# Optimization experiments

Hardware: AMD Instinct MI355X
Metric: run time of the kernel (lower is better)

Reference implementation:

```python
import jax, jax.numpy as jnp
import numpy as np
from jax import lax

HIDDEN = 7168
Q_LORA = 1536
N_HEAD = 64
HEAD_DIM = 128
ROPE_DIM = 64
TOPK = 2048
T = 4096
ROPE_BASE = 10000.0
LN_EPS = 1e-6
NEG_INF = -1e30


def _apply_rope_interleaved(x, cos, sin):
    # x: [..., ROPE_DIM], cos/sin broadcastable to [..., ROPE_DIM//2]
    x1 = x[..., 0::2]
    x2 = x[..., 1::2]
    o1 = x1 * cos - x2 * sin
    o2 = x1 * sin + x2 * cos
    out = jnp.stack([o1, o2], axis=-1)  # interleave back
    return out.reshape(x.shape)


def setup_inputs() -> dict:
    key = jax.random.key(0)
    ks = jax.random.split(key, 6)
    hidden_states = jax.random.normal(ks[0], (T, HIDDEN), dtype=jnp.float32)
    qr = jax.random.normal(ks[1], (T, Q_LORA), dtype=jnp.float32)
    positions = jnp.arange(T, dtype=jnp.int32)
    # learned parameters (stored [in, out] so fwd is x @ W)
    Wq_b = jax.random.normal(ks[2], (Q_LORA, N_HEAD * HEAD_DIM), dtype=jnp.float32) * 0.02
    Wk = jax.random.normal(ks[3], (HIDDEN, HEAD_DIM), dtype=jnp.float32) * 0.02
    Wproj = jax.random.normal(ks[4], (HIDDEN, N_HEAD), dtype=jnp.float32) * 0.02
    k_norm_gamma = jnp.ones((HEAD_DIM,), dtype=jnp.float32)
    k_norm_beta = jnp.zeros((HEAD_DIM,), dtype=jnp.float32)
    return {
        'hidden_states': hidden_states,
        'qr': qr,
        'positions': positions,
        'Wq_b': Wq_b,
        'Wk': Wk,
        'Wproj': Wproj,
        'k_norm_gamma': k_norm_gamma,
        'k_norm_beta': k_norm_beta,
    }


def _indexer_forward(hidden_states, qr, positions, Wq_b, Wk, Wproj, gamma, beta):
    # q projection: [T, n_head * head_dim] -> [T, H, D]
    q = (qr @ Wq_b).reshape(T, N_HEAD, HEAD_DIM)
    q_pe, q_nope = q[..., :ROPE_DIM], q[..., ROPE_DIM:]

    # k projection + LayerNorm (eps=1e-6)
    k = hidden_states @ Wk  # [T, D]
    mu = jnp.mean(k, axis=-1, keepdims=True)
    var = jnp.mean(jnp.square(k - mu), axis=-1, keepdims=True)
    k = (k - mu) * lax.rsqrt(var + LN_EPS) * gamma + beta
    k_pe, k_nope = k[..., :ROPE_DIM], k[..., ROPE_DIM:]

    # RoPE (interleaved / GPT-J style, as used by DeepSeek rotary)
    inv_freq = 1.0 / (ROPE_BASE ** (jnp.arange(0, ROPE_DIM, 2, dtype=jnp.float32) / ROPE_DIM))
    ang = positions.astype(jnp.float32)[:, None] * inv_freq[None, :]  # [T, R/2]
    cos, sin = jnp.cos(ang), jnp.sin(ang)
    q_pe = _apply_rope_interleaved(q_pe, cos[:, None, :], sin[:, None, :])  # [T, H, R]
    k_pe = _apply_rope_interleaved(k_pe, cos, sin)  # [T, R]

    q_full = jnp.concatenate([q_pe, q_nope], axis=-1)  # [T, H, D]
    k_full = jnp.concatenate([k_pe, k_nope], axis=-1)  # [T, D]

    # per-token per-head weights, scaled by head_dim**-0.5 * n_head**-0.5
    w = (hidden_states @ Wproj) * (HEAD_DIM ** -0.5) * (N_HEAD ** -0.5)  # [T, H]

    # lightning-indexer score: sum_h w[t,h] * relu(q[t,h,:] . k[s,:])
    # scan over heads so live intermediate is a single [T, T] matrix
    qh_all = jnp.transpose(q_full, (1, 0, 2))  # [H, T, D]
    wh_all = w.T  # [H, T]

    def body(acc, hw):
        qh, wh = hw  # [T, D], [T]
        acc = acc + wh[:, None] * jax.nn.relu(qh @ k_full.T)
        return acc, None

    scores, _ = lax.scan(body, jnp.zeros((T, T), dtype=jnp.float32), (qh_all, wh_all))

    # causal mask over key positions, then select top-k keys per query
    causal = positions[:, None] >= positions[None, :]
    masked = jnp.where(causal, scores, NEG_INF)
    topk_vals, topk_idx = lax.top_k(masked, TOPK)  # [T, TOPK]
    return topk_vals, topk_idx


def reference(hidden_states, qr, positions, Wq_b, Wk, Wproj, k_norm_gamma, k_norm_beta):
    return _indexer_forward(hidden_states, qr, positions, Wq_b, Wk, Wproj, k_norm_gamma, k_norm_beta)
```

## Files before the change

kernel.cpp:

```cpp
#include <hip/hip_runtime.h>
#include <stdint.h>

#define TT 4096
#define HID 7168
#define QL 1536
#define NH 64
#define HD 128
#define QD 8192
#define KTOP 2048
#define WSCALE 0.011048543456039806f

typedef _Float16 f16;
typedef uint16_t u16;
typedef unsigned u32;
typedef __attribute__((ext_vector_type(4))) float f32x4;
typedef __attribute__((ext_vector_type(16))) float f32x16;
typedef __attribute__((ext_vector_type(8))) _Float16 f16x8;
typedef __attribute__((ext_vector_type(4))) _Float16 f16x4;

__device__ __forceinline__ void lds_load16(const void* g, void* l) {
  __builtin_amdgcn_global_load_lds(
      (const __attribute__((address_space(1))) unsigned*)g,
      (__attribute__((address_space(3))) unsigned*)l, 16, 0, 0);
}

__device__ __forceinline__ u16 f16_bits(f16 h) {
  union { f16 h; u16 u; } c; c.h = h; return c.u;
}
__device__ __forceinline__ float f16_from_bits(u16 u) {
  union { u16 u; f16 h; } c; c.u = u; return (float)c.h;
}

__global__ void tcvt(const float* __restrict__ in, f16* __restrict__ out,
                     int R, int C, int ostride, int orow0) {
  __shared__ float tile[32][33];
  int cb = blockIdx.x * 32, rb = blockIdx.y * 32;
  int tx = threadIdx.x & 31, ty = threadIdx.x >> 5;
  for (int i = 0; i < 32; i += 8)
    tile[ty + i][tx] = in[(size_t)(rb + ty + i) * C + cb + tx];
  __syncthreads();
  for (int i = 0; i < 32; i += 8)
    out[(size_t)(cb + ty + i + orow0) * ostride + rb + tx] = (f16)tile[tx][ty + i];
}

__launch_bounds__(256, 2)
__global__ void gemm_q(const float* __restrict__ A, const f16* __restrict__ B, f16* __restrict__ C) {
  __shared__ __align__(16) f16 As[128 * 32];
  __shared__ __align__(16) f16 Bs[128 * 32];
  int tid = threadIdx.x, lane = tid & 63, wave = tid >> 6;
  int bm = blockIdx.y << 7, bn = blockIdx.x << 7;
  int wm = (wave & 1) << 6, wn = (wave >> 1) << 6;
  const f16* gb = B + (size_t)(bn + (tid >> 2)) * QL + (tid & 3) * 8;
  f16* lB = Bs + wave * 512;
  int ar = tid >> 3, ac = (tid & 7) * 4;
  f32x4 acc[4][4] = {};
  for (int k0 = 0; k0 < QL; k0 += 32) {
    __syncthreads();
#pragma unroll
    for (int i = 0; i < 4; i++) {
      float4 v = *(const float4*)(A + (size_t)(bm + ar + i * 32) * QL + k0 + ac);
      f16x4 h = {(f16)v.x, (f16)v.y, (f16)v.z, (f16)v.w};
      *(f16x4*)(As + (ar + i * 32) * 32 + ac) = h;
    }
    lds_load16(gb + k0, lB);
    lds_load16(gb + (size_t)64 * QL + k0, lB + 2048);
    __syncthreads();
    int ro = lane & 15, ko = (lane >> 4) << 3;
    f16x8 af[4], bf[4];
#pragma unroll
    for (int i = 0; i < 4; i++) af[i] = *(const f16x8*)(As + (wm + i * 16 + ro) * 32 + ko);
#pragma unroll
    for (int i = 0; i < 4; i++) bf[i] = *(const f16x8*)(Bs + (wn + i * 16 + ro) * 32 + ko);
#pragma unroll
    for (int mi = 0; mi < 4; mi++)
#pragma unroll
      for (int ni = 0; ni < 4; ni++)
        acc[mi][ni] = __builtin_amdgcn_mfma_f32_16x16x32_f16(af[mi], bf[ni], acc[mi][ni], 0, 0, 0);
  }
  int cr = (lane >> 4) << 2, cc = lane & 15;
#pragma unroll
  for (int mi = 0; mi < 4; mi++)
#pragma unroll
    for (int ni = 0; ni < 4; ni++) {
      int row = bm + wm + mi * 16 + cr;
      int col = bn + wn + ni * 16 + cc;
      f16* cp = C + (size_t)row * QD + col;
#pragma unroll
      for (int r = 0; r < 4; r++) cp[(size_t)r * QD] = (f16)acc[mi][ni][r];
    }
}

__launch_bounds__(256, 2)
__global__ void gemm_kw(const float* __restrict__ A, const f16* __restrict__ B,
                        float* __restrict__ kraw, float* __restrict__ wout) {
  __shared__ __align__(16) f16 As[64 * 64];
  __shared__ __align__(16) f16 Bs[64 * 64];
  int tid = threadIdx.x, lane = tid & 63, wave = tid >> 6;
  int bm = blockIdx.y << 6, bn = blockIdx.x << 6;
  int wm = (wave & 1) << 5, wn = (wave >> 1) << 5;
  const f16* gb = B + (size_t)(bn + (tid >> 3)) * HID + (tid & 7) * 8;
  f16* lB = Bs + wave * 512;
  int ar = tid >> 4, ac = (tid & 15) * 4;
  f32x4 acc[2][2] = {};
  for (int k0 = 0; k0 < HID; k0 += 64) {
    __syncthreads();
#pragma unroll
    for (int i = 0; i < 4; i++) {
      float4 v = *(const float4*)(A + (size_t)(bm + ar + i * 16) * HID + k0 + ac);
      f16x4 h = {(f16)v.x, (f16)v.y, (f16)v.z, (f16)v.w};
      *(f16x4*)(As + (ar + i * 16) * 64 + ac) = h;
    }
    lds_load16(gb + k0, lB);
    lds_load16(gb + (size_t)32 * HID + k0, lB + 2048);
    __syncthreads();
    int ro = lane & 15, ko = (lane >> 4) << 3;
    f16x8 af[2][2], bf[2][2];
#pragma unroll
    for (int i = 0; i < 2; i++)
#pragma unroll
      for (int kk = 0; kk < 2; kk++) {
        af[i][kk] = *(const f16x8*)(As + (wm + i * 16 + ro) * 64 + kk * 32 + ko);
        bf[i][kk] = *(const f16x8*)(Bs + (wn + i * 16 + ro) * 64 + kk * 32 + ko);
      }
#pragma unroll
    for (int mi = 0; mi < 2; mi++)
#pragma unroll
      for (int ni = 0; ni < 2; ni++)
#pragma unroll
        for (int kk = 0; kk < 2; kk++)
          acc[mi][ni] = __builtin_amdgcn_mfma_f32_16x16x32_f16(af[mi][kk], bf[ni][kk], acc[mi][ni], 0, 0, 0);
  }
  int cr = (lane >> 4) << 2, cc = lane & 15;
#pragma unroll
  for (int mi = 0; mi < 2; mi++)
#pragma unroll
    for (int ni = 0; ni < 2; ni++) {
      int row = bm + wm + mi * 16 + cr;
      int col = bn + wn + ni * 16 + cc;
#pragma unroll
      for (int r = 0; r < 4; r++) {
        float v = acc[mi][ni][r];
        int rr = row + r;
        if (col < HD) kraw[(size_t)rr * HD + col] = v;
        else          wout[(size_t)rr * NH + (col - HD)] = v * WSCALE;
      }
    }
}

__global__ void ln_rope(const float* __restrict__ kraw, const int* __restrict__ pos,
                        const float* __restrict__ gamma, const float* __restrict__ beta,
                        f16* __restrict__ k16) {
  int row = (blockIdx.x << 2) + (threadIdx.x >> 6);
  int lane = threadIdx.x & 63;
  const float* kr = kraw + (size_t)row * HD;
  float2 x = ((const float2*)kr)[lane];
  float s = x.x + x.y, s2 = x.x * x.x + x.y * x.y;
  for (int off = 32; off; off >>= 1) { s += __shfl_down(s, off); s2 += __shfl_down(s2, off); }
  s = __shfl(s, 0); s2 = __shfl(s2, 0);
  float mu = s * (1.f / 128.f);
  float var = s2 * (1.f / 128.f) - mu * mu;
  float inv = rsqrtf(var + 1e-6f);
  float y0 = (x.x - mu) * inv * gamma[lane * 2] + beta[lane * 2];
  float y1 = (x.y - mu) * inv * gamma[lane * 2 + 1] + beta[lane * 2 + 1];
  float o0 = y0, o1 = y1;
  if (lane < 32) {
    float p = (float)pos[row];
    float invf = exp2f(-(float)lane * 0.41524101185942813f);
    float ang = p * invf;
    float sn, cn;
    sincosf(ang, &sn, &cn);
    o0 = y0 * cn - y1 * sn;
    o1 = y0 * sn + y1 * cn;
  }
  k16[(size_t)row * HD + 2 * lane] = (f16)o0;
  k16[(size_t)row * HD + 2 * lane + 1] = (f16)o1;
}

template <int N>
__device__ __forceinline__ void sort_and_store(u32* key, int tid, int t, float* out) {
  constexpr int V = N / 256;
  u32 v[V];
#pragma unroll
  for (int r = 0; r < V; r += 4) {
    uint4 q4 = *(const uint4*)(key + tid * V + r);
    v[r] = ~q4.x; v[r + 1] = ~q4.y; v[r + 2] = ~q4.z; v[r + 3] = ~q4.w;
  }
#pragma unroll
  for (int k = 2; k <= N; k <<= 1) {
#pragma unroll
    for (int j = k >> 1; j > 0; j >>= 1) {
      if (j >= 64 * V) {
#pragma unroll
        for (int r = 0; r < V; r += 4) {
          uint4 q4 = {v[r], v[r + 1], v[r + 2], v[r + 3]};
          *(uint4*)(key + tid * V + r) = q4;
        }
        __syncthreads();
        for (int m = tid; m < N / 2; m += 256) {
          int i = ((m & ~(j - 1)) << 1) | (m & (j - 1));
          int l = i | j;
          bool up = ((i & k) == 0);
          u32 a = key[i], b = key[l];
          if (up ? (a > b) : (a < b)) { key[i] = b; key[l] = a; }
        }
        __syncthreads();
#pragma unroll
        for (int r = 0; r < V; r += 4) {
          uint4 q4 = *(const uint4*)(key + tid * V + r);
          v[r] = q4.x; v[r + 1] = q4.y; v[r + 2] = q4.z; v[r + 3] = q4.w;
        }
      } else if (j >= V) {
        int lanej = j / V;
        bool takeMin = (((tid & lanej) == 0) == (((tid * V) & k) == 0));
#pragma unroll
        for (int r = 0; r < V; r++) {
          u32 o = __shfl_xor(v[r], lanej, 64);
          u32 mn = min(v[r], o), mx = max(v[r], o);
          v[r] = takeMin ? mn : mx;
        }
      } else {
#pragma unroll
        for (int r = 0; r < V; r++) {
          if ((r & j) == 0) {
            bool up = (((tid * V + r) & k) == 0);
            u32 a = v[r], b = v[r | j];
            u32 mn = min(a, b), mx = max(a, b);
            v[r] = up ? mn : mx;
            v[r | j] = up ? mx : mn;
          }
        }
      }
    }
  }
  if (tid * V < KTOP) {
    float* ov = out + (size_t)t * KTOP + tid * V;
    float* oi = out + (size_t)TT * KTOP + (size_t)t * KTOP + tid * V;
#pragma unroll
    for (int r = 0; r < V; r++) {
      u32 kv = ~v[r];
      u32 mono = kv >> 16;
      float val;
      if (mono == 0u) {
        val = -1e30f;
      } else {
        u16 hb = (u16)((mono & 0x8000u) ? (mono ^ 0x8000u) : (mono ^ 0xFFFFu));
        val = f16_from_bits(hb);
      }
      ov[r] = val;
      oi[r] = (float)(0xFFFFu - (kv & 0xFFFFu));
    }
  }
}

__launch_bounds__(256, 3)
__global__ void scores_topk(const f16* __restrict__ q16, const f16* __restrict__ k16,
                            const float* __restrict__ w, const int* __restrict__ pos,
                            float* __restrict__ out) {
  int t = blockIdx.x;
  int tid = threadIdx.x, lane = tid & 63, wave = tid >> 6;
  __shared__ __align__(16) unsigned char smem[49408];
  f16* ks = (f16*)smem;
  f16* qk = (f16*)(smem + 32768);
  u32* key = (u32*)(smem + 32768);
  float* css = (float*)(smem + 49152);

  {
    const f16* qrow = q16 + (size_t)t * QD;
#pragma unroll
    for (int j = 0; j < 4; j++) {
      int u = j * 256 + tid;
      int kg = u >> 6, h = u & 63;
      lds_load16(qrow + h * 128 + kg * 8, qk + (size_t)(j * 256 + wave * 64) * 8);
    }
    if (tid < 32) {
      float invf = exp2f(-(float)tid * 0.41524101185942813f);
      float ang = (float)pos[t] * invf;
      float sn, cn;
      sincosf(ang, &sn, &cn);
      css[tid] = cn;
      css[32 + tid] = sn;
    }
  }
  __syncthreads();
#pragma unroll
  for (int i = 0; i < 8; i++) {
    int p = tid + (i << 8);
    int h = p >> 5, l = p & 31;
    int d = l * 2;
    int base = ((d >> 3) * 64 + h) * 8 + (d & 7);
    float q0 = (float)qk[base], q1 = (float)qk[base + 1];
    float cn = css[l], sn = css[32 + l];
    qk[base] = (f16)(q0 * cn - q1 * sn);
    qk[base + 1] = (f16)(q0 * sn + q1 * cn);
  }
  __syncthreads();
  f16x8 afr[2][8];
  {
    int m = lane & 31;
#pragma unroll
    for (int mi = 0; mi < 2; mi++)
#pragma unroll
      for (int kk = 0; kk < 8; kk++) {
        int kg = kk * 2 + (lane >> 5);
        afr[mi][kk] = *(const f16x8*)(qk + (size_t)(kg * 64 + mi * 32 + m) * 8);
      }
  }
  float wreg[32];
  {
    int hf = lane >> 5;
    const float* wr = w + (size_t)t * 64;
#pragma unroll
    for (int mi = 0; mi < 2; mi++)
#pragma unroll
      for (int r = 0; r < 16; r++)
        wreg[mi * 16 + r] = wr[mi * 32 + (r & 3) + ((r >> 2) << 3) + (hf << 2)];
  }
  __syncthreads();

  int nsort = (t <= 2047) ? 2048 : 4096;
  for (int s = tid; s < nsort; s += 256)
    key[s] = 0xFFFFu - (u32)s;

  int ntile = (t >> 7) + 1;
  int sw = wave << 5;
  for (int st = 0; st < ntile; st++) {
    int s0 = st << 7;
    __syncthreads();
    {
      const f16* kb = k16 + (size_t)s0 * HD;
#pragma unroll
      for (int j = 0; j < 8; j++) {
        int u = j * 256 + tid;
        int kg = u >> 7, s = u & 127;
        lds_load16(kb + s * HD + kg * 8, ks + (size_t)(j * 256 + wave * 64) * 8);
      }
    }
    __syncthreads();
    f32x16 acc0 = {}, acc1 = {};
    int nlo = lane & 31;
#pragma unroll
    for (int kk = 0; kk < 8; kk++) {
      int kg = kk * 2 + (lane >> 5);
      f16x8 bfr = *(const f16x8*)(ks + (size_t)(kg * 128 + sw + nlo) * 8);
      acc0 = __builtin_amdgcn_mfma_f32_32x32x16_f16(afr[0][kk], bfr, acc0, 0, 0, 0);
      acc1 = __builtin_amdgcn_mfma_f32_32x32x16_f16(afr[1][kk], bfr, acc1, 0, 0, 0);
    }
    float partial = 0.f;
#pragma unroll
    for (int r = 0; r < 16; r++) {
      partial += wreg[r] * fmaxf(acc0[r], 0.f);
      partial += wreg[16 + r] * fmaxf(acc1[r], 0.f);
    }
    partial += __shfl_xor(partial, 32);
    int s = s0 + sw + nlo;
    if (lane < 32 && s <= t) {
      if (!(partial == partial)) partial = 0.f;
      partial = fminf(fmaxf(partial, -60000.f), 60000.f);
      u16 hb = f16_bits((f16)partial);
      u32 m = (hb & 0x8000u) ? (u32)(hb ^ 0xFFFFu) : (u32)(hb | 0x8000u);
      key[s] = (m << 16) | (0xFFFFu - (u32)s);
    }
  }
  __syncthreads();

  if (t <= 2047) sort_and_store<2048>(key, tid, t, out);
  else           sort_and_store<4096>(key, tid, t, out);
}

extern "C" void kernel_launch(void* const* d_in, const int* in_sizes, int n_in,
                              void* d_out, int out_size, void* d_ws, size_t ws_size,
                              hipStream_t stream) {
  const float* hs = (const float*)d_in[0];
  const float* qr = (const float*)d_in[1];
  const int* pos = (const int*)d_in[2];
  const float* Wq = (const float*)d_in[3];
  const float* Wk = (const float*)d_in[4];
  const float* Wp = (const float*)d_in[5];
  const float* gamma = (const float*)d_in[6];
  const float* beta = (const float*)d_in[7];
  char* ws = (char*)d_ws;
  float* kraw = (float*)ws;
  float* wsc = (float*)(ws + 2097152);
  f16* k16 = (f16*)(ws + 3145728);
  f16* kwT = (f16*)(ws + 4194304);
  f16* wqT = (f16*)(ws + 6946816);
  f16* q16 = (f16*)(ws + 32112640);

  tcvt<<<dim3(256, 48), dim3(256), 0, stream>>>(Wq, wqT, QL, QD, QL, 0);
  tcvt<<<dim3(4, 224), dim3(256), 0, stream>>>(Wk, kwT, HID, HD, HID, 0);
  tcvt<<<dim3(2, 224), dim3(256), 0, stream>>>(Wp, kwT, HID, NH, HID, HD);
  gemm_kw<<<dim3(3, 64), dim3(256), 0, stream>>>(hs, kwT, kraw, wsc);
  ln_rope<<<dim3(1024), dim3(256), 0, stream>>>(kraw, pos, gamma, beta, k16);
  gemm_q<<<dim3(64, 32), dim3(256), 0, stream>>>(qr, wqT, q16);
  scores_topk<<<dim3(4096), dim3(256), 0, stream>>>(q16, k16, wsc, pos, (float*)d_out);
}
```

Measured before the change: 846.5 us.

## Split fused scores+topk into tiled score GEMM, separate RoPE, and top-k kernels

The per-query fused kernel, which reloaded every K tile for each query row, is replaced by three kernels. A separate pass applies RoPE to q in place. A 2D-tiled kernel then computes 32 queries by 256 keys, holding K fragments in registers, double-buffering per-head q slices through LDS, and writing causal f16 scores to a packed triangular buffer. A final top-k kernel reads those scores back and runs the existing bitonic sort. This raises K reuse and MFMA density, at the cost of extra launches and a global round trip for the score matrix. The score buffer reuses the workspace region of the transposed weights.

```diff
diff --git a/kernel.cpp b/kernel.cpp
--- a/kernel.cpp
+++ b/kernel.cpp
@@ -29,6 +29,11 @@
 }
 __device__ __forceinline__ float f16_from_bits(u16 u) {
   union { u16 u; f16 h; } c; c.u = u; return (float)c.h;
+}
+
+__device__ __forceinline__ size_t soff(int t) {
+  int b = t >> 7, r = t & 127;
+  return (size_t)128u * ((size_t)(b + 1) * (size_t)(64 * b + r));
 }
 
 __global__ void tcvt(const float* __restrict__ in, f16* __restrict__ out,
@@ -176,6 +181,127 @@
   k16[(size_t)row * HD + 2 * lane + 1] = (f16)o1;
 }
 
+__global__ void rope_q(f16* __restrict__ q16, const int* __restrict__ pos) {
+  int t = blockIdx.x, tid = threadIdx.x;
+  __shared__ float cs[64];
+  if (tid < 32) {
+    float invf = exp2f(-(float)tid * 0.41524101185942813f);
+    float ang = (float)pos[t] * invf;
+    float sn, cn;
+    sincosf(ang, &sn, &cn);
+    cs[tid] = cn;
+    cs[32 + tid] = sn;
+  }
+  __syncthreads();
+  f16* row = q16 + (size_t)t * QD;
+#pragma unroll
+  for (int it = 0; it < 2; it++) {
+    int u = it * 256 + tid;
+    int h = u >> 3, c = u & 7;
+    f16* p = row + h * HD + c * 8;
+    f16x8 v = *(f16x8*)p;
+#pragma unroll
+    for (int j = 0; j < 4; j++) {
+      int l = c * 4 + j;
+      float cn = cs[l], sn = cs[32 + l];
+      float x = (float)v[2 * j], y = (float)v[2 * j + 1];
+      v[2 * j] = (f16)(x * cn - y * sn);
+      v[2 * j + 1] = (f16)(x * sn + y * cn);
+    }
+    *(f16x8*)p = v;
+  }
+}
+
+__launch_bounds__(256, 3)
+__global__ void scores2(const f16* __restrict__ q16, const f16* __restrict__ k16,
+                        const float* __restrict__ w, f16* __restrict__ S) {
+  int kt0 = blockIdx.x << 8;
+  int qt0 = blockIdx.y << 5;
+  if (kt0 > qt0 + 31) return;
+  int tid = threadIdx.x, l = tid & 63, wid = tid >> 6;
+  int q = l & 31, half = l >> 5;
+  __shared__ __align__(16) f16 smem_q[8192];
+  __shared__ float w_lds[2048];
+
+  for (int i = tid; i < 2048; i += 256) {
+    int hh = i & 63, qq = i >> 6;
+    w_lds[hh * 32 + qq] = w[(size_t)(qt0 + qq) * NH + hh];
+  }
+  f16x8 kfr[2][8];
+  {
+    const f16* kb = k16 + (size_t)(kt0 + wid * 64 + q) * HD + half * 8;
+#pragma unroll
+    for (int mt = 0; mt < 2; mt++)
+#pragma unroll
+      for (int kk = 0; kk < 8; kk++)
+        kfr[mt][kk] = *(const f16x8*)(kb + mt * 32 * HD + kk * 16);
+  }
+  const f16* qbase = q16 + (size_t)qt0 * QD;
+#pragma unroll
+  for (int p = 0; p < 2; p++) {
+    int u = p * 256 + tid;
+    lds_load16(qbase + (size_t)(u & 31) * QD + (u >> 5) * 8, smem_q + u * 8);
+  }
+  f32x16 s0 = {}, s1 = {};
+  __syncthreads();
+
+  for (int h = 0; h < NH; h++) {
+    if (h < NH - 1) {
+      const f16* src = qbase + (h + 1) * HD;
+      f16* dst = smem_q + ((h + 1) & 1) * 4096;
+#pragma unroll
+      for (int p = 0; p < 2; p++) {
+        int u = p * 256 + tid;
+        lds_load16(src + (size_t)(u & 31) * QD + (u >> 5) * 8, dst + u * 8);
+      }
+    }
+    const f16* qb = smem_q + (h & 1) * 4096;
+    f32x16 a0 = {}, a1 = {};
+#pragma unroll
+    for (int kk = 0; kk < 8; kk++) {
+      f16x8 qf = *(const f16x8*)(qb + ((kk * 2 + half) * 32 + q) * 8);
+      a0 = __builtin_amdgcn_mfma_f32_32x32x16_f16(kfr[0][kk], qf, a0, 0, 0, 0);
+      a1 = __builtin_amdgcn_mfma_f32_32x32x16_f16(kfr[1][kk], qf, a1, 0, 0, 0);
+    }
+    float wv = w_lds[h * 32 + q];
+#pragma unroll
+    for (int r = 0; r < 16; r++) {
+      s0[r] += wv * fmaxf(a0[r], 0.f);
+      s1[r] += wv * fmaxf(a1[r], 0.f);
+    }
+    __syncthreads();
+  }
+
+  f16* st = smem_q;
+#pragma unroll
+  for (int mt = 0; mt < 2; mt++)
+#pragma unroll
+    for (int r = 0; r < 16; r++) {
+      int m = (r & 3) + ((r >> 2) << 3) + half * 4;
+      int sl = wid * 64 + mt * 32 + m;
+      float v = mt ? s1[r] : s0[r];
+      if (!(v == v)) v = 0.f;
+      v = fminf(fmaxf(v, -60000.f), 60000.f);
+      u32 byte = (u32)(q * 512 + sl * 2) ^ (u32)((q & 7) << 4);
+      *(f16*)((char*)st + byte) = (f16)v;
+    }
+  __syncthreads();
+  {
+    int rq = tid >> 3, c = tid & 7;
+    int t = qt0 + rq;
+    size_t base = soff(t) + (size_t)kt0;
+    bool hi = (t - kt0) >= 128;
+#pragma unroll
+    for (int j = 0; j < 4; j++) {
+      if (c < 4 || hi) {
+        u32 byte = (u32)(rq * 512 + c * 64 + j * 16) ^ (u32)((rq & 7) << 4);
+        uint4 v = *(uint4*)((char*)st + byte);
+        *(uint4*)(S + base + c * 32 + j * 8) = v;
+      }
+    }
+  }
+}
+
 template <int N>
 __device__ __forceinline__ void sort_and_store(u32* key, int tid, int t, float* out) {
   constexpr int V = N / 256;
@@ -252,117 +378,31 @@
   }
 }
 
-__launch_bounds__(256, 3)
-__global__ void scores_topk(const f16* __restrict__ q16, const f16* __restrict__ k16,
-                            const float* __restrict__ w, const int* __restrict__ pos,
-                            float* __restrict__ out) {
-  int t = blockIdx.x;
-  int tid = threadIdx.x, lane = tid & 63, wave = tid >> 6;
-  __shared__ __align__(16) unsigned char smem[49408];
-  f16* ks = (f16*)smem;
-  f16* qk = (f16*)(smem + 32768);
-  u32* key = (u32*)(smem + 32768);
-  float* css = (float*)(smem + 49152);
-
-  {
-    const f16* qrow = q16 + (size_t)t * QD;
-#pragma unroll
-    for (int j = 0; j < 4; j++) {
-      int u = j * 256 + tid;
-      int kg = u >> 6, h = u & 63;
-      lds_load16(qrow + h * 128 + kg * 8, qk + (size_t)(j * 256 + wave * 64) * 8);
-    }
-    if (tid < 32) {
-      float invf = exp2f(-(float)tid * 0.41524101185942813f);
-      float ang = (float)pos[t] * invf;
-      float sn, cn;
-      sincosf(ang, &sn, &cn);
-      css[tid] = cn;
-      css[32 + tid] = sn;
+__launch_bounds__(256, 4)
+__global__ void topk_k(const f16* __restrict__ S, float* __restrict__ out) {
+  int t = blockIdx.x, tid = threadIdx.x;
+  __shared__ __align__(16) u32 key[4096];
+  size_t base = soff(t);
+  int nsort = (t <= 2047) ? 2048 : 4096;
+  const uint4* src = (const uint4*)(S + base);
+  for (int i = tid; i < (nsort >> 3); i += 256) {
+    uint4 v4 = src[i];
+    u32 ww[4] = {v4.x, v4.y, v4.z, v4.w};
+#pragma unroll
+    for (int j = 0; j < 8; j++) {
+      int s = i * 8 + j;
+      u32 kk;
+      if (s > t) {
+        kk = 0xFFFFu - (u32)s;
+      } else {
+        u16 hb = (u16)(ww[j >> 1] >> ((j & 1) * 16));
+        u32 mono = (hb & 0x8000u) ? (u32)(hb ^ 0xFFFFu) : (u32)(hb | 0x8000u);
+        kk = (mono << 16) | (0xFFFFu - (u32)s);
+      }
+      key[s] = kk;
     }
   }
   __syncthreads();
-#pragma unroll
-  for (int i = 0; i < 8; i++) {
-    int p = tid + (i << 8);
-    int h = p >> 5, l = p & 31;
-    int d = l * 2;
-    int base = ((d >> 3) * 64 + h) * 8 + (d & 7);
-    float q0 = (float)qk[base], q1 = (float)qk[base + 1];
-    float cn = css[l], sn = css[32 + l];
-    qk[base] = (f16)(q0 * cn - q1 * sn);
-    qk[base + 1] = (f16)(q0 * sn + q1 * cn);
-  }
-  __syncthreads();
-  f16x8 afr[2][8];
-  {
-    int m = lane & 31;
-#pragma unroll
-    for (int mi = 0; mi < 2; mi++)
-#pragma unroll
-      for (int kk = 0; kk < 8; kk++) {
-        int kg = kk * 2 + (lane >> 5);
-        afr[mi][kk] = *(const f16x8*)(qk + (size_t)(kg * 64 + mi * 32 + m) * 8);
-      }
-  }
-  float wreg[32];
-  {
-    int hf = lane >> 5;
-    const float* wr = w + (size_t)t * 64;
-#pragma unroll
-    for (int mi = 0; mi < 2; mi++)
-#pragma unroll
-      for (int r = 0; r < 16; r++)
-        wreg[mi * 16 + r] = wr[mi * 32 + (r & 3) + ((r >> 2) << 3) + (hf << 2)];
-  }
-  __syncthreads();
-
-  int nsort = (t <= 2047) ? 2048 : 4096;
-  for (int s = tid; s < nsort; s += 256)
-    key[s] = 0xFFFFu - (u32)s;
-
-  int ntile = (t >> 7) + 1;
-  int sw = wave << 5;
-  for (int st = 0; st < ntile; st++) {
-    int s0 = st << 7;
-    __syncthreads();
-    {
-      const f16* kb = k16 + (size_t)s0 * HD;
-#pragma unroll
-      for (int j = 0; j < 8; j++) {
-        int u = j * 256 + tid;
-        int kg = u >> 7, s = u & 127;
-        lds_load16(kb + s * HD + kg * 8, ks + (size_t)(j * 256 + wave * 64) * 8);
-      }
-    }
-    __syncthreads();
-    f32x16 acc0 = {}, acc1 = {};
-    int nlo = lane & 31;
-#pragma unroll
-    for (int kk = 0; kk < 8; kk++) {
-      int kg = kk * 2 + (lane >> 5);
-      f16x8 bfr = *(const f16x8*)(ks + (size_t)(kg * 128 + sw + nlo) * 8);
-      acc0 = __builtin_amdgcn_mfma_f32_32x32x16_f16(afr[0][kk], bfr, acc0, 0, 0, 0);
-      acc1 = __builtin_amdgcn_mfma_f32_32x32x16_f16(afr[1][kk], bfr, acc1, 0, 0, 0);
-    }
-    float partial = 0.f;
-#pragma unroll
-    for (int r = 0; r < 16; r++) {
-      partial += wreg[r] * fmaxf(acc0[r], 0.f);
-      partial += wreg[16 + r] * fmaxf(acc1[r], 0.f);
-    }
-    partial += __shfl_xor(partial, 32);
-    int s = s0 + sw + nlo;
-    if (lane < 32 && s <= t) {
-      if (!(partial == partial)) partial = 0.f;
-      partial = fminf(fmaxf(partial, -60000.f), 60000.f);
-      u16 hb = f16_bits((f16)partial);
-      u32 m = (hb & 0x8000u) ? (u32)(hb ^ 0xFFFFu) : (u32)(hb | 0x8000u);
-      key[s] = (m << 16) | (0xFFFFu - (u32)s);
-    }
-  }
-  __syncthreads();
-
   if (t <= 2047) sort_and_store<2048>(key, tid, t, out);
   else           sort_and_store<4096>(key, tid, t, out);
 }
@@ -385,6 +425,7 @@
   f16* kwT = (f16*)(ws + 4194304);
   f16* wqT = (f16*)(ws + 6946816);
   f16* q16 = (f16*)(ws + 32112640);
+  f16* S = (f16*)(ws + 4194304);
 
   tcvt<<<dim3(256, 48), dim3(256), 0, stream>>>(Wq, wqT, QL, QD, QL, 0);
   tcvt<<<dim3(4, 224), dim3(256), 0, stream>>>(Wk, kwT, HID, HD, HID, 0);
@@ -392,5 +433,7 @@
   gemm_kw<<<dim3(3, 64), dim3(256), 0, stream>>>(hs, kwT, kraw, wsc);
   ln_rope<<<dim3(1024), dim3(256), 0, stream>>>(kraw, pos, gamma, beta, k16);
   gemm_q<<<dim3(64, 32), dim3(256), 0, stream>>>(qr, wqT, q16);
-  scores_topk<<<dim3(4096), dim3(256), 0, stream>>>(q16, k16, wsc, pos, (float*)d_out);
-}
+  rope_q<<<dim3(4096), dim3(256), 0, stream>>>(q16, pos);
+  scores2<<<dim3(16, 128), dim3(256), 0, stream>>>(q16, k16, wsc, S);
+  topk_k<<<dim3(4096), dim3(256), 0, stream>>>(S, (float*)d_out);
+}
```

Measured after the change: 860.1 us. No clear change (+1.6%).
